# Performance work log

Hardware: AMD Instinct MI355X
Metric: run time of the kernel (lower is better)

Reference implementation:

```python
import jax, jax.numpy as jnp
import numpy as np

N_NODES = 50000
N_EDGES = 1600000
N_GRAPHS = 2048
DIM = 133
EPS = 1e-5


def gcn_conv(x, W, b, row, col, n_nodes):
    # PyG GCNConv: h = x @ W; add self-loops; sym-normalized scatter-add; + b
    h = x @ W  # [N, D]
    loops = jnp.arange(n_nodes, dtype=row.dtype)
    r = jnp.concatenate([row, loops])
    c = jnp.concatenate([col, loops])
    deg = jax.ops.segment_sum(jnp.ones_like(c, dtype=h.dtype), c, num_segments=n_nodes)
    dinv = jnp.where(deg > 0, jax.lax.rsqrt(deg), 0.0)
    norm = dinv[r] * dinv[c]  # [E+N]
    msg = h[r] * norm[:, None]  # gather + scale
    out = jax.ops.segment_sum(msg, c, num_segments=n_nodes)
    return out + b


def batchnorm_eval(x, gamma, beta, rm, rv):
    return (x - rm) * jax.lax.rsqrt(rv + EPS) * gamma + beta


def setup_inputs() -> dict:
    key = jax.random.key(0)
    ks = jax.random.split(key, 8)
    x = jax.random.normal(ks[0], (N_NODES, DIM), dtype=jnp.float32)
    edge_index = jax.random.randint(ks[1], (2, N_EDGES), 0, N_NODES, dtype=jnp.int64)
    batch = jnp.sort(jax.random.randint(ks[2], (N_NODES,), 0, N_GRAPHS, dtype=jnp.int64))
    s = 1.0 / np.sqrt(DIM)
    W1 = jax.random.uniform(ks[3], (DIM, DIM), jnp.float32, -s, s)
    W2 = jax.random.uniform(ks[4], (DIM, DIM), jnp.float32, -s, s)
    b1 = jnp.zeros((DIM,), jnp.float32)
    b2 = jnp.zeros((DIM,), jnp.float32)
    g1 = jnp.ones((DIM,), jnp.float32); beta1 = jnp.zeros((DIM,), jnp.float32)
    rm1 = jax.random.normal(ks[5], (DIM,), jnp.float32) * 0.1
    rv1 = jnp.ones((DIM,), jnp.float32)
    g2 = jnp.ones((DIM,), jnp.float32); beta2 = jnp.zeros((DIM,), jnp.float32)
    rm2 = jax.random.normal(ks[6], (DIM,), jnp.float32) * 0.1
    rv2 = jnp.ones((DIM,), jnp.float32)
    return {"x": x, "edge_index": edge_index, "batch": batch,
            "W1": W1, "b1": b1, "W2": W2, "b2": b2,
            "g1": g1, "beta1": beta1, "rm1": rm1, "rv1": rv1,
            "g2": g2, "beta2": beta2, "rm2": rm2, "rv2": rv2}


def reference(x, edge_index, batch, W1, b1, W2, b2,
              g1, beta1, rm1, rv1, g2, beta2, rm2, rv2):
    row, col = edge_index[0], edge_index[1]
    h = gcn_conv(x, W1, b1, row, col, N_NODES)
    h = jax.nn.relu(h)
    h = batchnorm_eval(h, g1, beta1, rm1, rv1)  # eval-mode BN; dropout is identity in eval
    h = gcn_conv(h, W2, b2, row, col, N_NODES)
    h = jax.nn.relu(h)
    h = batchnorm_eval(h, g2, beta2, rm2, rv2)
    # global mean pool per graph
    sums = jax.ops.segment_sum(h, batch, num_segments=N_GRAPHS)
    cnts = jax.ops.segment_sum(jnp.ones((N_NODES,), h.dtype), batch, num_segments=N_GRAPHS)
    return sums / jnp.maximum(cnts, 1.0)[:, None]
```

## Files before the change

kernel.cpp:

```cpp
#include <hip/hip_runtime.h>

#define N_NODES  50000
#define N_ROWS   50048
#define N_EDGES  1600000
#define N_GRAPHS 2048
#define DIM      133
#define HSTR     136
#define YSTR     160
#define EPSV     1e-5f
#define NRANGE   16
#define RSPAN    3125
#define NSLICE   64
#define BUCKCAP  110000
#define EPB      1563

typedef __attribute__((ext_vector_type(8))) short bf16x8;
typedef __attribute__((ext_vector_type(4))) float f32x4;

__device__ __forceinline__ float blo(unsigned u) { return __uint_as_float(u << 16); }
__device__ __forceinline__ float bhi(unsigned u) { return __uint_as_float(u & 0xFFFF0000u); }
__device__ __forceinline__ unsigned short f2bf(float x) {
    unsigned v = __float_as_uint(x);
    return (unsigned short)((v + 0x7FFFu + ((v >> 16) & 1u)) >> 16);
}
__device__ __forceinline__ unsigned packbf(float a, float b) {
    return (unsigned)f2bf(a) | ((unsigned)f2bf(b) << 16);
}


__global__ __launch_bounds__(256) void k_part(const int* __restrict__ row,
                                              const int* __restrict__ col,
                                              int* __restrict__ bcnt,
                                              unsigned* __restrict__ buckets)
{
    __shared__ int cnt[NRANGE];
    __shared__ int cur[NRANGE];
    int e0 = blockIdx.x * EPB;
    if (threadIdx.x < NRANGE) cnt[threadIdx.x] = 0;
    __syncthreads();
    int e1 = min(e0 + EPB, N_EDGES);
    for (int e = e0 + threadIdx.x; e < e1; e += 256)
        atomicAdd(&cnt[col[e] / RSPAN], 1);
    __syncthreads();
    if (threadIdx.x < NRANGE)
        cur[threadIdx.x] = atomicAdd(&bcnt[threadIdx.x], cnt[threadIdx.x]);
    __syncthreads();
    for (int e = e0 + threadIdx.x; e < e1; e += 256) {
        int c = col[e];
        int r = c / RSPAN;
        int p = atomicAdd(&cur[r], 1);
        buckets[(size_t)r * BUCKCAP + p] =
            ((unsigned)row[e] << 12) | (unsigned)(c - r * RSPAN);
    }
}

__global__ __launch_bounds__(256) void k_count2(const unsigned* __restrict__ buckets,
                                                const int* __restrict__ bcnt,
                                                int* __restrict__ deg2)
{
    __shared__ int hist[RSPAN];
    int r = blockIdx.x & (NRANGE - 1);
    int s = blockIdx.x >> 4;
    int lo = r * RSPAN;
    for (int i = threadIdx.x; i < RSPAN; i += 256) hist[i] = 0;
    __syncthreads();
    int n = bcnt[r];
    int chunk = (n + NSLICE - 1) / NSLICE;
    int e0 = s * chunk, e1 = min(e0 + chunk, n);
    const unsigned* b = buckets + (size_t)r * BUCKCAP;
    for (int e = e0 + threadIdx.x; e < e1; e += 256)
        atomicAdd(&hist[b[e] & 0xFFFu], 1);
    __syncthreads();
    for (int i = threadIdx.x; i < RSPAN; i += 256)
        deg2[(size_t)s * N_NODES + lo + i] = hist[i];
}

__device__ __forceinline__ void w2bf_one(const float* __restrict__ W,
                                         unsigned short* __restrict__ Wbf, int idx)
{
    int j    = idx & 7;
    int lane = (idx >> 3) & 63;
    int kc   = (idx >> 9) % 5;
    int t    = idx / (8 * 64 * 5);
    int k = kc * 32 + (lane >> 4) * 8 + j;
    int n = t * 16 + (lane & 15);
    float v = (k < DIM && n < DIM) ? W[k * DIM + n] : 0.f;
    Wbf[idx] = f2bf(v);
}

#define X2BF_BLOCKS 15625

__global__ __launch_bounds__(256) void k_prep(const float* __restrict__ x,
                                              unsigned* __restrict__ Abf,
                                              const float* __restrict__ W1,
                                              const float* __restrict__ W2,
                                              unsigned short* __restrict__ Wbf1,
                                              unsigned short* __restrict__ Wbf2,
                                              const int* __restrict__ batch,
                                              float* __restrict__ inv_cnt)
{
    if (blockIdx.x < X2BF_BLOCKS) {
        int idx = blockIdx.x * 256 + threadIdx.x;
        if (idx >= N_NODES * 80) return;
        int r  = idx / 80;
        int c2 = (idx - r * 80) * 2;
        float a = (c2     < DIM) ? x[(size_t)r * DIM + c2]     : 0.f;
        float b = (c2 + 1 < DIM) ? x[(size_t)r * DIM + c2 + 1] : 0.f;
        Abf[idx] = packbf(a, b);
        return;
    }
    int tid = (blockIdx.x - X2BF_BLOCKS) * 256 + threadIdx.x;
    if (tid < 23040) {
        w2bf_one(W1, Wbf1, tid);
    } else if (tid < 46080) {
        w2bf_one(W2, Wbf2, tid - 23040);
    } else if (tid < 46080 + N_GRAPHS) {
        int g = tid - 46080;
        int a0 = 0, b0 = N_NODES;
        while (a0 < b0) { int m = (a0 + b0) >> 1; if (batch[m] < g) a0 = m + 1; else b0 = m; }
        int a1 = a0, b1 = N_NODES;
        while (a1 < b1) { int m = (a1 + b1) >> 1; if (batch[m] < g + 1) a1 = m + 1; else b1 = m; }
        inv_cnt[g] = 1.0f / (float)max(a1 - a0, 1);
    }
}

__global__ __launch_bounds__(256) void k_scan1(const int* __restrict__ deg2,
                                               float* __restrict__ dinv,
                                               int* __restrict__ offs,
                                               int* __restrict__ bsum)
{
    __shared__ int sd[256];
    int t = threadIdx.x;
    int idx = blockIdx.x * 256 + t;
    int v = 0;
    if (idx < N_NODES) {
        for (int s = 0; s < NSLICE; s++) v += deg2[(size_t)s * N_NODES + idx];
        dinv[idx] = rsqrtf((float)v + 1.0f);
    }
    sd[t] = v; __syncthreads();
    for (int o = 1; o < 256; o <<= 1) {
        int add = (t >= o) ? sd[t - o] : 0;
        __syncthreads();
        sd[t] += add;
        __syncthreads();
    }
    if (idx < N_NODES) offs[idx] = sd[t] - v;
    if (t == 255) bsum[blockIdx.x] = sd[255];
}

__global__ __launch_bounds__(256) void k_scan2(const int* __restrict__ bsum,
                                               int* __restrict__ boff, int nb)
{
    __shared__ int sd[256];
    int t = threadIdx.x;
    int v = (t < nb) ? bsum[t] : 0;
    sd[t] = v; __syncthreads();
    for (int o = 1; o < 256; o <<= 1) {
        int add = (t >= o) ? sd[t - o] : 0;
        __syncthreads();
        sd[t] += add;
        __syncthreads();
    }
    boff[t] = sd[t] - v;
}

__global__ __launch_bounds__(256) void k_scan3C(int* __restrict__ offs,
                                                const int* __restrict__ boff,
                                                int* __restrict__ deg2)
{
    int idx = blockIdx.x * 256 + threadIdx.x;
    if (idx < N_NODES) {
        int off = offs[idx] + boff[blockIdx.x];
        offs[idx] = off;
        int run = off;
        for (int s = 0; s < NSLICE; s++) {
            int d = deg2[(size_t)s * N_NODES + idx];
            deg2[(size_t)s * N_NODES + idx] = run;
            run += d;
        }
    } else if (idx == N_NODES) {
        offs[N_NODES] = N_EDGES;
    }
}

__global__ __launch_bounds__(256) void k_fill2(const unsigned* __restrict__ buckets,
                                               const int* __restrict__ bcnt,
                                               const int* __restrict__ offs2,
                                               const float* __restrict__ dinv,
                                               unsigned* __restrict__ csr)
{
    __shared__ int cur[RSPAN];
    int r = blockIdx.x & (NRANGE - 1);
    int s = blockIdx.x >> 4;
    int lo = r * RSPAN;
    for (int i = threadIdx.x; i < RSPAN; i += 256)
        cur[i] = offs2[(size_t)s * N_NODES + lo + i];
    __syncthreads();
    int n = bcnt[r];
    int chunk = (n + NSLICE - 1) / NSLICE;
    int e0 = s * chunk, e1 = min(e0 + chunk, n);
    const unsigned* b = buckets + (size_t)r * BUCKCAP;
    for (int e = e0 + threadIdx.x; e < e1; e += 256) {
        unsigned v = b[e];
        int src = (int)(v >> 12);
        int p = atomicAdd(&cur[v & 0xFFFu], 1);
        csr[p] = ((unsigned)src << 16) | (unsigned)f2bf(dinv[src]);
    }
}

__global__ __launch_bounds__(256) void k_gemm_mfma(const unsigned short* __restrict__ A,
                                                   const unsigned short* __restrict__ Wbf,
                                                   unsigned short* __restrict__ H, int M)
{
    int wave = threadIdx.x >> 6, lane = threadIdx.x & 63;
    int quad = lane >> 4, l16 = lane & 15;
    int m = blockIdx.x * 64 + wave * 16 + l16;

    const bf16x8* Arow = (const bf16x8*)(A + (size_t)m * YSTR);
    const bf16x8* Bq   = (const bf16x8*)Wbf;

    f32x4 acc[9] = {};
#pragma unroll
    for (int kc = 0; kc < 5; kc++) {
        bf16x8 af = Arow[kc * 4 + quad];
#pragma unroll
        for (int t = 0; t < 9; t++) {
            bf16x8 bfr = Bq[(t * 5 + kc) * 64 + lane];
            acc[t] = __builtin_amdgcn_mfma_f32_16x16x32_bf16(af, bfr, acc[t], 0, 0, 0);
        }
    }

    int gr0 = blockIdx.x * 64 + wave * 16 + quad * 4;
#pragma unroll
    for (int t = 0; t < 9; t++) {
        int c = t * 16 + l16;
#pragma unroll
        for (int reg = 0; reg < 4; reg++) {
            int gr = gr0 + reg;
            if (gr < M && c < HSTR) {
                float v = (c < DIM) ? acc[t][reg] : 0.f;
                H[(size_t)gr * HSTR + c] = f2bf(v);
            }
        }
    }
}


template <bool FINAL>
__global__ __launch_bounds__(256) void k_agg(const unsigned short* __restrict__ h,
                                             const int* __restrict__ offs,
                                             const unsigned* __restrict__ csr,
                                             const float* __restrict__ dinv,
                                             const float* __restrict__ bias,
                                             const float* __restrict__ gam,
                                             const float* __restrict__ bet,
                                             const float* __restrict__ rmean,
                                             const float* __restrict__ rvar,
                                             unsigned short* __restrict__ y,
                                             const int* __restrict__ batch,
                                             const float* __restrict__ inv_cnt,
                                             float* __restrict__ outp)
{
    int node = __builtin_amdgcn_readfirstlane(blockIdx.x * 4 + (threadIdx.x >> 6));
    if (node >= N_NODES) return;
    int lane = threadIdx.x & 63;
    int l2 = lane & 3;

    float di = dinv[node];
    const unsigned* hrow = (const unsigned*)(h + (size_t)node * HSTR);
    unsigned p0 = hrow[lane];
    unsigned p1 = hrow[64 + l2];
    float2 a0; a0.x = di * blo(p0); a0.y = di * bhi(p0);
    float2 a1; a1.x = di * blo(p1); a1.y = di * bhi(p1);

    int s0 = offs[node], s1 = offs[node + 1];
    int e = s0;
    for (; e + 8 <= s1; e += 8) {
        unsigned rec[8];
#pragma unroll
        for (int u = 0; u < 8; u++) rec[u] = csr[e + u];
        unsigned q0[8], q1[8];
#pragma unroll
        for (int u = 0; u < 8; u++) {
            const unsigned* hr = (const unsigned*)(h + (size_t)(rec[u] >> 16) * HSTR);
            q0[u] = hr[lane];
            q1[u] = hr[64 + l2];
        }
#pragma unroll
        for (int u = 0; u < 8; u++) {
            float w = __uint_as_float(rec[u] << 16);
            a0.x += w * blo(q0[u]); a0.y += w * bhi(q0[u]);
            a1.x += w * blo(q1[u]); a1.y += w * bhi(q1[u]);
        }
    }
    for (; e < s1; e++) {
        unsigned rec = csr[e];
        float w = __uint_as_float(rec << 16);
        const unsigned* hr = (const unsigned*)(h + (size_t)(rec >> 16) * HSTR);
        unsigned q0 = hr[lane];
        unsigned q1 = hr[64 + l2];
        a0.x += w * blo(q0); a0.y += w * bhi(q0);
        a1.x += w * blo(q1); a1.y += w * bhi(q1);
    }

    float ic = 0.f; int bg = 0;
    if (FINAL) { bg = batch[node]; ic = inv_cnt[bg]; }

    {
        int c = 2 * lane;
        float va = di * a0.x + bias[c];
        va = fmaxf(va, 0.f);
        va = (va - rmean[c]) * (gam[c] * rsqrtf(rvar[c] + EPSV)) + bet[c];
        int c1 = c + 1;
        float vb = di * a0.y + bias[c1];
        vb = fmaxf(vb, 0.f);
        vb = (vb - rmean[c1]) * (gam[c1] * rsqrtf(rvar[c1] + EPSV)) + bet[c1];
        if (FINAL) {
            atomicAdd(&outp[(size_t)bg * DIM + c],  va * ic);
            atomicAdd(&outp[(size_t)bg * DIM + c1], vb * ic);
        } else {
            ((unsigned*)(y + (size_t)node * YSTR))[lane] = packbf(va, vb);
        }
    }
    if (lane < 16) {
        float va = 0.f, vb = 0.f;
        if (lane < 4) {
            int c = 128 + 2 * l2;
            if (c < DIM) {
                va = di * a1.x + bias[c];
                va = fmaxf(va, 0.f);
                va = (va - rmean[c]) * (gam[c] * rsqrtf(rvar[c] + EPSV)) + bet[c];
            }
            int c1 = c + 1;
            if (c1 < DIM) {
                vb = di * a1.y + bias[c1];
                vb = fmaxf(vb, 0.f);
                vb = (vb - rmean[c1]) * (gam[c1] * rsqrtf(rvar[c1] + EPSV)) + bet[c1];
            }
            if (FINAL) {
                if (c  < DIM) atomicAdd(&outp[(size_t)bg * DIM + c],  va * ic);
                if (c1 < DIM) atomicAdd(&outp[(size_t)bg * DIM + c1], vb * ic);
            }
        }
        if (!FINAL)
            ((unsigned*)(y + (size_t)node * YSTR))[64 + lane] = packbf(va, vb);
    }
}


extern "C" void kernel_launch(void* const* d_in, const int* in_sizes, int n_in,
                              void* d_out, int out_size, void* d_ws, size_t ws_size,
                              hipStream_t stream)
{
    const float* x   = (const float*)d_in[0];
    const int*   ei  = (const int*)d_in[1];
    const int*   bat = (const int*)d_in[2];
    const float* W1  = (const float*)d_in[3];
    const float* b1  = (const float*)d_in[4];
    const float* W2  = (const float*)d_in[5];
    const float* b2  = (const float*)d_in[6];
    const float* g1  = (const float*)d_in[7];
    const float* be1 = (const float*)d_in[8];
    const float* rm1 = (const float*)d_in[9];
    const float* rv1 = (const float*)d_in[10];
    const float* g2  = (const float*)d_in[11];
    const float* be2 = (const float*)d_in[12];
    const float* rm2 = (const float*)d_in[13];
    const float* rv2 = (const float*)d_in[14];
    float* outp = (float*)d_out;
    char* ws = (char*)d_ws;

    int*   bcnt    = (int*)  (ws + 0);
    int*   offs    = (int*)  (ws + 200000);
    float* dinv    = (float*)(ws + 400016);
    float* inv_cnt = (float*)(ws + 600016);
    int*   bsum    = (int*)  (ws + 608208);
    int*   boff    = (int*)  (ws + 609232);
    unsigned* csr  = (unsigned*)(ws + 610256);
    unsigned short* Wbf1 = (unsigned short*)(ws + 7010256);
    unsigned short* Wbf2 = (unsigned short*)(ws + 7056336);
    unsigned short* Abf  = (unsigned short*)(ws + 7102416);
    unsigned short* Y1   = Abf;
    unsigned short* Hb   = (unsigned short*)(ws + 23117776);
    unsigned* buckets = (unsigned*)(ws + 23117776);
    int*      deg2    = (int*)    (ws + 30157776);

    hipMemsetAsync(bcnt, 0, 64, stream);
    hipMemsetAsync(d_out, 0, (size_t)out_size * 4, stream);

    const int* row = ei;
    const int* col = ei + N_EDGES;

    int nbl = (N_NODES + 255) / 256;

    k_part  <<<dim3(1024), dim3(256), 0, stream>>>(row, col, bcnt, buckets);
    k_prep  <<<dim3(X2BF_BLOCKS + 189), dim3(256), 0, stream>>>(x, (unsigned*)Abf,
                                                                W1, W2, Wbf1, Wbf2,
                                                                bat, inv_cnt);
    k_count2<<<dim3(NSLICE * NRANGE), dim3(256), 0, stream>>>(buckets, bcnt, deg2);
    k_scan1 <<<dim3(nbl), dim3(256), 0, stream>>>(deg2, dinv, offs, bsum);
    k_scan2 <<<dim3(1),   dim3(256), 0, stream>>>(bsum, boff, nbl);
    k_scan3C<<<dim3(nbl), dim3(256), 0, stream>>>(offs, boff, deg2);
    k_fill2 <<<dim3(NSLICE * NRANGE), dim3(256), 0, stream>>>(buckets, bcnt, deg2, dinv, csr);

    int gbl = N_ROWS / 64;
    k_gemm_mfma<<<dim3(gbl), dim3(256), 0, stream>>>(Abf, Wbf1, Hb, N_NODES);
    k_agg<false><<<dim3(N_NODES / 4), dim3(256), 0, stream>>>(Hb, offs, csr, dinv,
                                                              b1, g1, be1, rm1, rv1,
                                                              Y1, nullptr, nullptr, nullptr);
    k_gemm_mfma<<<dim3(gbl), dim3(256), 0, stream>>>(Y1, Wbf2, Hb, N_NODES);
    k_agg<true><<<dim3(N_NODES / 4), dim3(256), 0, stream>>>(Hb, offs, csr, dinv,
                                                             b2, g2, be2, rm2, rv2,
                                                             nullptr, bat, inv_cnt, outp);
}
```

Before: 357.7 us.

## Split H into 128-col main and 8-col tail arrays; batch final-layer pooling per wave

The GEMM output H is stored as two arrays: a 256-byte-aligned main block of 128 bf16 columns and a separate 8-column tail. This makes each neighbor-row gather in aggregation line-aligned instead of using a 136-element stride that straddles cache lines. The final aggregation has each wave process 10 consecutive nodes, accumulating the pooled sum in registers and issuing atomics only when the graph id changes. That cuts global atomic traffic into the output, but gives fewer, longer-running waves in the last layer, which may hurt latency hiding.

```diff
diff --git a/kernel.cpp b/kernel.cpp
--- a/kernel.cpp
+++ b/kernel.cpp
@@ -5,7 +5,8 @@
 #define N_EDGES  1600000
 #define N_GRAPHS 2048
 #define DIM      133
-#define HSTR     136
+#define HMSTR    128
+#define HTSTR    8
 #define YSTR     160
 #define EPSV     1e-5f
 #define NRANGE   16
@@ -13,6 +14,7 @@
 #define NSLICE   64
 #define BUCKCAP  110000
 #define EPB      1563
+#define NPN      10
 
 typedef __attribute__((ext_vector_type(8))) short bf16x8;
 typedef __attribute__((ext_vector_type(4))) float f32x4;
@@ -210,7 +212,8 @@
 
 __global__ __launch_bounds__(256) void k_gemm_mfma(const unsigned short* __restrict__ A,
                                                    const unsigned short* __restrict__ Wbf,
-                                                   unsigned short* __restrict__ H, int M)
+                                                   unsigned short* __restrict__ Hmain,
+                                                   unsigned short* __restrict__ Htail, int M)
 {
     int wave = threadIdx.x >> 6, lane = threadIdx.x & 63;
     int quad = lane >> 4, l16 = lane & 15;
@@ -237,17 +240,101 @@
 #pragma unroll
         for (int reg = 0; reg < 4; reg++) {
             int gr = gr0 + reg;
-            if (gr < M && c < HSTR) {
-                float v = (c < DIM) ? acc[t][reg] : 0.f;
-                H[(size_t)gr * HSTR + c] = f2bf(v);
+            if (gr < M) {
+                if (c < HMSTR) {
+                    Hmain[(size_t)gr * HMSTR + c] = f2bf(acc[t][reg]);
+                } else if (c < HMSTR + HTSTR) {
+                    float v = (c < DIM) ? acc[t][reg] : 0.f;
+                    Htail[(size_t)gr * HTSTR + (c - HMSTR)] = f2bf(v);
+                }
             }
         }
     }
 }
 
 
+__device__ __forceinline__ void agg_row(const unsigned short* __restrict__ hmain,
+                                        const unsigned short* __restrict__ htail,
+                                        const int* __restrict__ offs,
+                                        const unsigned* __restrict__ csr,
+                                        const float* __restrict__ dinv,
+                                        const float* __restrict__ bias,
+                                        const float* __restrict__ gam,
+                                        const float* __restrict__ bet,
+                                        const float* __restrict__ rmean,
+                                        const float* __restrict__ rvar,
+                                        int node, int lane, int l2,
+                                        float& va, float& vb, float& ta, float& tb)
+{
+    const unsigned* hm = (const unsigned*)hmain;
+    const unsigned* ht = (const unsigned*)htail;
+
+    float di = dinv[node];
+    unsigned pw0 = hm[((size_t)node << 6) + lane];
+    unsigned pw1 = ht[((unsigned)node << 2) + l2];
+    float2 a0; a0.x = di * blo(pw0); a0.y = di * bhi(pw0);
+    float2 a1; a1.x = di * blo(pw1); a1.y = di * bhi(pw1);
+
+    int s0 = offs[node], s1 = offs[node + 1];
+    int e = s0;
+    for (; e + 8 <= s1; e += 8) {
+        unsigned rec[8];
+#pragma unroll
+        for (int u = 0; u < 8; u++) rec[u] = csr[e + u];
+        unsigned q0[8], q1[8];
+#pragma unroll
+        for (int u = 0; u < 8; u++) {
+            unsigned src = rec[u] >> 16;
+            q0[u] = hm[((size_t)src << 6) + lane];
+            q1[u] = ht[(src << 2) + l2];
+        }
+#pragma unroll
+        for (int u = 0; u < 8; u++) {
+            float w = __uint_as_float(rec[u] << 16);
+            a0.x += w * blo(q0[u]); a0.y += w * bhi(q0[u]);
+            a1.x += w * blo(q1[u]); a1.y += w * bhi(q1[u]);
+        }
+    }
+    for (; e < s1; e++) {
+        unsigned rec = csr[e];
+        unsigned src = rec >> 16;
+        float w = __uint_as_float(rec << 16);
+        unsigned q0 = hm[((size_t)src << 6) + lane];
+        unsigned q1 = ht[(src << 2) + l2];
+        a0.x += w * blo(q0); a0.y += w * bhi(q0);
+        a1.x += w * blo(q1); a1.y += w * bhi(q1);
+    }
+
+    {
+        int c = 2 * lane;
+        float v = di * a0.x + bias[c];
+        v = fmaxf(v, 0.f);
+        va = (v - rmean[c]) * (gam[c] * rsqrtf(rvar[c] + EPSV)) + bet[c];
+        int c1 = c + 1;
+        v = di * a0.y + bias[c1];
+        v = fmaxf(v, 0.f);
+        vb = (v - rmean[c1]) * (gam[c1] * rsqrtf(rvar[c1] + EPSV)) + bet[c1];
+    }
+    ta = 0.f; tb = 0.f;
+    if (lane < 4) {
+        int c = 128 + 2 * l2;
+        if (c < DIM) {
+            float v = di * a1.x + bias[c];
+            v = fmaxf(v, 0.f);
+            ta = (v - rmean[c]) * (gam[c] * rsqrtf(rvar[c] + EPSV)) + bet[c];
+        }
+        int c1 = c + 1;
+        if (c1 < DIM) {
+            float v = di * a1.y + bias[c1];
+            v = fmaxf(v, 0.f);
+            tb = (v - rmean[c1]) * (gam[c1] * rsqrtf(rvar[c1] + EPSV)) + bet[c1];
+        }
+    }
+}
+
 template <bool FINAL>
-__global__ __launch_bounds__(256) void k_agg(const unsigned short* __restrict__ h,
+__global__ __launch_bounds__(256) void k_agg(const unsigned short* __restrict__ hmain,
+                                             const unsigned short* __restrict__ htail,
                                              const int* __restrict__ offs,
                                              const unsigned* __restrict__ csr,
                                              const float* __restrict__ dinv,
@@ -261,89 +348,59 @@
                                              const float* __restrict__ inv_cnt,
                                              float* __restrict__ outp)
 {
-    int node = __builtin_amdgcn_readfirstlane(blockIdx.x * 4 + (threadIdx.x >> 6));
-    if (node >= N_NODES) return;
     int lane = threadIdx.x & 63;
     int l2 = lane & 3;
 
-    float di = dinv[node];
-    const unsigned* hrow = (const unsigned*)(h + (size_t)node * HSTR);
-    unsigned p0 = hrow[lane];
-    unsigned p1 = hrow[64 + l2];
-    float2 a0; a0.x = di * blo(p0); a0.y = di * bhi(p0);
-    float2 a1; a1.x = di * blo(p1); a1.y = di * bhi(p1);
-
-    int s0 = offs[node], s1 = offs[node + 1];
-    int e = s0;
-    for (; e + 8 <= s1; e += 8) {
-        unsigned rec[8];
-#pragma unroll
-        for (int u = 0; u < 8; u++) rec[u] = csr[e + u];
-        unsigned q0[8], q1[8];
-#pragma unroll
-        for (int u = 0; u < 8; u++) {
-            const unsigned* hr = (const unsigned*)(h + (size_t)(rec[u] >> 16) * HSTR);
-            q0[u] = hr[lane];
-            q1[u] = hr[64 + l2];
-        }
-#pragma unroll
-        for (int u = 0; u < 8; u++) {
-            float w = __uint_as_float(rec[u] << 16);
-            a0.x += w * blo(q0[u]); a0.y += w * bhi(q0[u]);
-            a1.x += w * blo(q1[u]); a1.y += w * bhi(q1[u]);
-        }
-    }
-    for (; e < s1; e++) {
-        unsigned rec = csr[e];
-        float w = __uint_as_float(rec << 16);
-        const unsigned* hr = (const unsigned*)(h + (size_t)(rec >> 16) * HSTR);
-        unsigned q0 = hr[lane];
-        unsigned q1 = hr[64 + l2];
-        a0.x += w * blo(q0); a0.y += w * bhi(q0);
-        a1.x += w * blo(q1); a1.y += w * bhi(q1);
-    }
-
-    float ic = 0.f; int bg = 0;
-    if (FINAL) { bg = batch[node]; ic = inv_cnt[bg]; }
-
+    if (!FINAL) {
+        int node = __builtin_amdgcn_readfirstlane(blockIdx.x * 4 + (threadIdx.x >> 6));
+        if (node >= N_NODES) return;
+        float va, vb, ta, tb;
+        agg_row(hmain, htail, offs, csr, dinv, bias, gam, bet, rmean, rvar,
+                node, lane, l2, va, vb, ta, tb);
+        ((unsigned*)(y + (size_t)node * YSTR))[lane] = packbf(va, vb);
+        if (lane < 16)
+            ((unsigned*)(y + (size_t)node * YSTR))[64 + lane] =
+                (lane < 4) ? packbf(ta, tb) : 0u;
+        return;
+    }
+
+    int node0 = __builtin_amdgcn_readfirstlane((blockIdx.x * 4 + (threadIdx.x >> 6)) * NPN);
+    if (node0 >= N_NODES) return;
+    int nend = min(node0 + NPN, N_NODES);
+
+    float p0x = 0.f, p0y = 0.f, p1x = 0.f, p1y = 0.f;
+    int curg = batch[node0];
+
+    for (int node = node0; node < nend; node++) {
+        int bg = batch[node];
+        if (bg != curg) {
+            float ic = inv_cnt[curg];
+            int c = 2 * lane;
+            atomicAdd(&outp[(size_t)curg * DIM + c],     p0x * ic);
+            atomicAdd(&outp[(size_t)curg * DIM + c + 1], p0y * ic);
+            if (lane < 4) {
+                int ct = 128 + 2 * l2;
+                if (ct     < DIM) atomicAdd(&outp[(size_t)curg * DIM + ct],     p1x * ic);
+                if (ct + 1 < DIM) atomicAdd(&outp[(size_t)curg * DIM + ct + 1], p1y * ic);
+            }
+            p0x = p0y = p1x = p1y = 0.f;
+            curg = bg;
+        }
+        float va, vb, ta, tb;
+        agg_row(hmain, htail, offs, csr, dinv, bias, gam, bet, rmean, rvar,
+                node, lane, l2, va, vb, ta, tb);
+        p0x += va; p0y += vb; p1x += ta; p1y += tb;
+    }
     {
+        float ic = inv_cnt[curg];
         int c = 2 * lane;
-        float va = di * a0.x + bias[c];
-        va = fmaxf(va, 0.f);
-        va = (va - rmean[c]) * (gam[c] * rsqrtf(rvar[c] + EPSV)) + bet[c];
-        int c1 = c + 1;
-        float vb = di * a0.y + bias[c1];
-        vb = fmaxf(vb, 0.f);
-        vb = (vb - rmean[c1]) * (gam[c1] * rsqrtf(rvar[c1] + EPSV)) + bet[c1];
-        if (FINAL) {
-            atomicAdd(&outp[(size_t)bg * DIM + c],  va * ic);
-            atomicAdd(&outp[(size_t)bg * DIM + c1], vb * ic);
-        } else {
-            ((unsigned*)(y + (size_t)node * YSTR))[lane] = packbf(va, vb);
-        }
-    }
-    if (lane < 16) {
-        float va = 0.f, vb = 0.f;
+        atomicAdd(&outp[(size_t)curg * DIM + c],     p0x * ic);
+        atomicAdd(&outp[(size_t)curg * DIM + c + 1], p0y * ic);
         if (lane < 4) {
-            int c = 128 + 2 * l2;
-            if (c < DIM) {
-                va = di * a1.x + bias[c];
-                va = fmaxf(va, 0.f);
-                va = (va - rmean[c]) * (gam[c] * rsqrtf(rvar[c] + EPSV)) + bet[c];
-            }
-            int c1 = c + 1;
-            if (c1 < DIM) {
-                vb = di * a1.y + bias[c1];
-                vb = fmaxf(vb, 0.f);
-                vb = (vb - rmean[c1]) * (gam[c1] * rsqrtf(rvar[c1] + EPSV)) + bet[c1];
-            }
-            if (FINAL) {
-                if (c  < DIM) atomicAdd(&outp[(size_t)bg * DIM + c],  va * ic);
-                if (c1 < DIM) atomicAdd(&outp[(size_t)bg * DIM + c1], vb * ic);
-            }
-        }
-        if (!FINAL)
-            ((unsigned*)(y + (size_t)node * YSTR))[64 + lane] = packbf(va, vb);
+            int ct = 128 + 2 * l2;
+            if (ct     < DIM) atomicAdd(&outp[(size_t)curg * DIM + ct],     p1x * ic);
+            if (ct + 1 < DIM) atomicAdd(&outp[(size_t)curg * DIM + ct + 1], p1y * ic);
+        }
     }
 }
 
@@ -381,9 +438,10 @@
     unsigned short* Wbf2 = (unsigned short*)(ws + 7056336);
     unsigned short* Abf  = (unsigned short*)(ws + 7102416);
     unsigned short* Y1   = Abf;
-    unsigned short* Hb   = (unsigned short*)(ws + 23117776);
-    unsigned* buckets = (unsigned*)(ws + 23117776);
-    int*      deg2    = (int*)    (ws + 30157776);
+    unsigned short* Hm   = (unsigned short*)(ws + 23118080);
+    unsigned short* Ht   = (unsigned short*)(ws + 35930368);
+    unsigned* buckets = (unsigned*)(ws + 23118080);
+    int*      deg2    = (int*)    (ws + 30158080);
 
     hipMemsetAsync(bcnt, 0, 64, stream);
     hipMemsetAsync(d_out, 0, (size_t)out_size * 4, stream);
@@ -404,12 +462,13 @@
     k_fill2 <<<dim3(NSLICE * NRANGE), dim3(256), 0, stream>>>(buckets, bcnt, deg2, dinv, csr);
 
     int gbl = N_ROWS / 64;
-    k_gemm_mfma<<<dim3(gbl), dim3(256), 0, stream>>>(Abf, Wbf1, Hb, N_NODES);
-    k_agg<false><<<dim3(N_NODES / 4), dim3(256), 0, stream>>>(Hb, offs, csr, dinv,
+    k_gemm_mfma<<<dim3(gbl), dim3(256), 0, stream>>>(Abf, Wbf1, Hm, Ht, N_NODES);
+    k_agg<false><<<dim3(N_NODES / 4), dim3(256), 0, stream>>>(Hm, Ht, offs, csr, dinv,
                                                               b1, g1, be1, rm1, rv1,
                                                               Y1, nullptr, nullptr, nullptr);
-    k_gemm_mfma<<<dim3(gbl), dim3(256), 0, stream>>>(Y1, Wbf2, Hb, N_NODES);
-    k_agg<true><<<dim3(N_NODES / 4), dim3(256), 0, stream>>>(Hb, offs, csr, dinv,
-                                                             b2, g2, be2, rm2, rv2,
-                                                             nullptr, bat, inv_cnt, outp);
-}
+    k_gemm_mfma<<<dim3(gbl), dim3(256), 0, stream>>>(Y1, Wbf2, Hm, Ht, N_NODES);
+    int fbl = (N_NODES + 4 * NPN - 1) / (4 * NPN);
+    k_agg<true><<<dim3(fbl), dim3(256), 0, stream>>>(Hm, Ht, offs, csr, dinv,
+                                                     b2, g2, be2, rm2, rv2,
+                                                     nullptr, bat, inv_cnt, outp);
+}
```

New measurement: 326.0 us. 8.9% less time.
